# Kernel optimization log

Measured on AMD Instinct MI355X. Metric: run time of the kernel, lower is better.

Reference implementation:

```python
import jax, jax.numpy as jnp
import numpy as np
from jax import lax

B, C, T_IN = 512, 22, 1001   # input width includes the subject-id column
K, KS, P = 40, 25, 100       # num_kernels, kernel_size, pool_size
S, NOUT = 9, 4               # num_subjects, n_outputs
BN_EPS = 1e-5


def setup_inputs() -> dict:
    key = jax.random.key(0)
    ks = jax.random.split(key, 6)
    x = jax.random.normal(ks[0], (B, C, T_IN), dtype=jnp.float32)
    # subject ids in 1..9 encoded as id*1e6 at x[:, 0, -1] (as in the torch module)
    sid = jax.random.randint(ks[1], (B,), 1, S + 1)
    x = x.at[:, 0, -1].set(sid.astype(jnp.float32) * 1e6)
    W = 0.05 * jax.random.normal(ks[2], (S, K, C, KS), dtype=jnp.float32)
    b = 0.05 * jax.random.normal(ks[3], (S, K), dtype=jnp.float32)
    gamma = jnp.ones((K,), dtype=jnp.float32)
    beta = jnp.zeros((K,), dtype=jnp.float32)
    fc_in = K * ((T_IN - 1 - KS + 1) // P)  # 40 * 9 = 360
    fc_w = 0.05 * jax.random.normal(ks[4], (NOUT, fc_in), dtype=jnp.float32)
    fc_b = jnp.zeros((NOUT,), dtype=jnp.float32)
    return {"x": x, "W": W, "b": b, "gamma": gamma, "beta": beta,
            "fc_w": fc_w, "fc_b": fc_b}


def reference(x, W, b, gamma, beta, fc_w, fc_b):
    # decode per-sample subject routing id (0-based into stacked weights)
    sid = (x[:, 0, -1] / 1e6).astype(jnp.int32) - 1        # [B]
    xs = x[:, :, :-1]                                      # [B, C, T]
    Wg = W[sid]                                            # [B, K, C, KS] gathered expert weights
    bg = b[sid]                                            # [B, K]

    # per-sample 1D valid conv with its own expert weights (batched via vmap)
    def conv1(xi, wi):  # xi: [C, T], wi: [K, C, KS]
        return lax.conv_general_dilated(xi[None], wi, (1,), 'VALID',
                                        dimension_numbers=('NCH', 'OIH', 'NCH'))[0]

    y = jax.vmap(conv1)(xs, Wg) + bg[:, :, None]           # [B, K, To]
    y = jax.nn.elu(y)

    # BatchNorm2d in training mode: batch statistics over (B, spatial), biased var
    mean = y.mean(axis=(0, 2))
    var = y.var(axis=(0, 2))
    y = (y - mean[None, :, None]) * (gamma / jnp.sqrt(var + BN_EPS))[None, :, None] \
        + beta[None, :, None]

    # AvgPool over non-overlapping windows of size P (stride = P, floor)
    To = y.shape[-1]
    nw = To // P
    y = y[..., : nw * P].reshape(y.shape[0], K, nw, P).mean(axis=-1)  # [B, K, nw]

    y = y.reshape(y.shape[0], -1)          # [B, K*nw]; dropout is identity in eval
    return y @ fc_w.T + fc_b               # [B, NOUT]
```

## Files before the change

### kernel.cpp

```cpp
#include <hip/hip_runtime.h>
#include <hip/hip_bf16.h>

#define B_ 512
#define C_ 22
#define TIN 1001
#define K_ 40
#define KS_ 25
#define TO 976
#define P_ 100
#define NW 9
#define NOUT 4
#define FCIN 360
#define NBLK 512

#define XTR 1056
#define LDS_TOTAL (XTR * 64)
#define NPAD 48
#define WB_ELEM_S (KS_ * NPAD * 32)

typedef __attribute__((ext_vector_type(8))) short bf16x8;
typedef __attribute__((ext_vector_type(4))) float f32x4;
typedef __attribute__((ext_vector_type(4))) int i32x4;

__device__ __forceinline__ float waveReduceSum(float v) {
#pragma unroll
  for (int m = 32; m >= 1; m >>= 1) v += __shfl_xor(v, m, 64);
  return v;
}

__device__ __forceinline__ unsigned short f2bf(float f) {
  __hip_bfloat16 h = __float2bfloat16(f);
  return *reinterpret_cast<unsigned short*>(&h);
}

__global__ __launch_bounds__(192) void wconv_kernel(const float* __restrict__ W,
                                                    unsigned short* __restrict__ WBg) {
  const int s = blockIdx.x / KS_;
  const int j = blockIdx.x % KS_;
  const int n = threadIdx.x >> 2;
  const int q = threadIdx.x & 3;
  union {
    unsigned short u[8];
    i32x4 v;
  } pk;
#pragma unroll
  for (int e = 0; e < 8; ++e) {
    const int c = q * 8 + e;
    float v = 0.f;
    if (n < K_ && c < C_) v = W[(((size_t)s * K_ + n) * C_ + c) * KS_ + j];
    pk.u[e] = f2bf(v);
  }
  *(i32x4*)(WBg + ((size_t)(s * KS_ + j) * NPAD + n) * 32 + q * 8) = pk.v;
}

#define MFMA24(A, Bv)                                                          \
  do {                                                                         \
    _Pragma("unroll") for (int nt_ = 0; nt_ < 3; ++nt_) {                      \
      _Pragma("unroll") for (int m_ = 0; m_ < 8; ++m_) {                       \
        acc[m_][nt_] =                                                         \
            __builtin_amdgcn_mfma_f32_16x16x32_bf16(A[m_], Bv[nt_], acc[m_][nt_], 0, 0, 0); \
      }                                                                        \
    }                                                                          \
  } while (0)

__global__ __launch_bounds__(512, 2) void conv_kernel(
    const float* __restrict__ x, const unsigned short* __restrict__ WBg,
    const float* __restrict__ bias, float* __restrict__ pooled,
    float* __restrict__ part_sum, float* __restrict__ part_sq) {
  extern __shared__ __align__(16) char sm[];
  const int b = blockIdx.x;
  const int tid = threadIdx.x;

  int s = (int)rintf(x[(size_t)b * (C_ * TIN) + (TIN - 1)] * 1e-6f) - 1;
  s = __builtin_amdgcn_readfirstlane(min(max(s, 0), 8));

  {
    const float* xb = x + (size_t)b * (C_ * TIN);
    for (int task = tid; task < 4 * XTR; task += 512) {
      const int q = task / XTR;
      const int t = task - q * XTR;
      const int lq = q ^ ((t >> 1) & 3);
      union {
        unsigned short u[8];
        i32x4 v;
      } pk;
#pragma unroll
      for (int e = 0; e < 8; ++e) {
        const int c = lq * 8 + e;
        float v = 0.f;
        if (c < C_ && t < TIN - 1) v = xb[c * TIN + t];
        pk.u[e] = f2bf(v);
      }
      *(i32x4*)(sm + t * 64 + q * 16) = pk.v;
    }
  }
  __syncthreads();

  const int lane = tid & 63;
  const int wv = tid >> 6;
  const int l15 = lane & 15;
  const int lg = lane >> 4;
  const int rb = wv * 128;
  const int tb = rb + l15;

  const unsigned short* WBs = WBg + (size_t)s * WB_ELEM_S + (l15 * 32 + lg * 8);

  f32x4 acc[8][3];
#pragma unroll
  for (int m = 0; m < 8; ++m)
#pragma unroll
    for (int nt = 0; nt < 3; ++nt) acc[m][nt] = (f32x4){0.f, 0.f, 0.f, 0.f};

  bf16x8 A0[8], A1[8], B0[3], B1[3];

#define LDA(J, A)                                                              \
  do {                                                                         \
    const int t_ = tb + (J);                                                   \
    const char* ap_ = sm + t_ * 64 + ((lg ^ ((t_ >> 1) & 3)) << 4);            \
    _Pragma("unroll") for (int m_ = 0; m_ < 8; ++m_) {                         \
      A[m_] = *(const bf16x8*)(ap_ + m_ * 1024);                               \
    }                                                                          \
  } while (0)

#define LDB(J, Bv)                                                             \
  do {                                                                         \
    const unsigned short* bp_ = WBs + (size_t)(J)*1536;                        \
    _Pragma("unroll") for (int nt_ = 0; nt_ < 3; ++nt_) {                      \
      Bv[nt_] = *(const bf16x8*)(bp_ + nt_ * 512);                             \
    }                                                                          \
  } while (0)

  LDA(0, A0);
  LDB(0, B0);
  for (int j = 0; j < 24; j += 2) {
    LDA(j + 1, A1);
    LDB(j + 1, B1);
    MFMA24(A0, B0);
    LDA(j + 2, A0);
    LDB(j + 2, B0);
    MFMA24(A1, B1);
  }
  MFMA24(A0, B0);

  float bv[3];
#pragma unroll
  for (int nt = 0; nt < 3; ++nt) {
    const int k = nt * 16 + l15;
    bv[nt] = bias[s * K_ + (k < K_ ? k : 0)];
  }
  const int wlo = rb / P_;
  const int base100 = wlo * P_;
  float sY[3] = {0.f, 0.f, 0.f}, sY2[3] = {0.f, 0.f, 0.f};
  float p0[3] = {0.f, 0.f, 0.f}, p1[3] = {0.f, 0.f, 0.f}, p2[3] = {0.f, 0.f, 0.f};
#pragma unroll
  for (int m = 0; m < 8; ++m) {
#pragma unroll
    for (int i = 0; i < 4; ++i) {
      const int t = rb + m * 16 + lg * 4 + i;
      const bool valid = (t < TO);
      const bool pool = (t < NW * P_);
      const int d = t - base100;
#pragma unroll
      for (int nt = 0; nt < 3; ++nt) {
        const float v = acc[m][nt][i] + bv[nt];
        const float y = v > 0.f ? v : expm1f(v);
        if (valid) {
          sY[nt] += y;
          sY2[nt] += y * y;
          if (pool) {
            if (d < P_)
              p0[nt] += y;
            else if (d < 2 * P_)
              p1[nt] += y;
            else
              p2[nt] += y;
          }
        }
      }
    }
  }
  float* red = (float*)sm;
  __syncthreads();
#pragma unroll
  for (int nt = 0; nt < 3; ++nt) {
#pragma unroll
    for (int r = 16; r <= 32; r <<= 1) {
      p0[nt] += __shfl_xor(p0[nt], r, 64);
      p1[nt] += __shfl_xor(p1[nt], r, 64);
      p2[nt] += __shfl_xor(p2[nt], r, 64);
      sY[nt] += __shfl_xor(sY[nt], r, 64);
      sY2[nt] += __shfl_xor(sY2[nt], r, 64);
    }
    const int k = nt * 16 + l15;
    if (lane < 16 && k < K_) {
      float* pb = pooled + (size_t)b * FCIN + k * NW;
      if (p0[nt] != 0.f) atomicAdd(&pb[wlo], p0[nt]);
      if (wlo + 1 <= NW - 1 && p1[nt] != 0.f) atomicAdd(&pb[wlo + 1], p1[nt]);
      if (wlo + 2 <= NW - 1 && p2[nt] != 0.f) atomicAdd(&pb[wlo + 2], p2[nt]);
      red[k * 8 + wv] = sY[nt];
      red[K_ * 8 + k * 8 + wv] = sY2[nt];
    }
  }
  __syncthreads();
  if (tid < K_) {
    float a = 0.f, q = 0.f;
#pragma unroll
    for (int i = 0; i < 8; ++i) {
      a += red[tid * 8 + i];
      q += red[K_ * 8 + tid * 8 + i];
    }
    part_sum[(size_t)tid * NBLK + b] = a;
    part_sq[(size_t)tid * NBLK + b] = q;
  }
}

__global__ __launch_bounds__(256) void stats_kernel(
    const float* __restrict__ part_sum, const float* __restrict__ part_sq,
    const float* __restrict__ gamma, const float* __restrict__ beta,
    float* __restrict__ ss) {
  const int k = blockIdx.x;
  float s = 0.f, q = 0.f;
  for (int i = threadIdx.x; i < NBLK; i += 256) {
    s += part_sum[(size_t)k * NBLK + i];
    q += part_sq[(size_t)k * NBLK + i];
  }
  s = waveReduceSum(s);
  q = waveReduceSum(q);
  __shared__ float ls[4], lq[4];
  const int wave = threadIdx.x >> 6, lane = threadIdx.x & 63;
  if (lane == 0) {
    ls[wave] = s;
    lq[wave] = q;
  }
  __syncthreads();
  if (threadIdx.x == 0) {
    const float S = ls[0] + ls[1] + ls[2] + ls[3];
    const float Q = lq[0] + lq[1] + lq[2] + lq[3];
    const float N = (float)B_ * (float)TO;
    const float mean = S / N;
    const float var = Q / N - mean * mean;
    const float sc = gamma[k] / sqrtf(var + 1e-5f);
    ss[k] = sc;
    ss[K_ + k] = beta[k] - mean * sc;
  }
}

__global__ __launch_bounds__(256) void fc_kernel(
    const float* __restrict__ pooled, const float* __restrict__ ss,
    const float* __restrict__ fc_w, const float* __restrict__ fc_b,
    float* __restrict__ out) {
  const int bb = blockIdx.x;
  const int n = threadIdx.x >> 6;
  const int lane = threadIdx.x & 63;
  float acc = 0.f;
  for (int i = lane; i < FCIN; i += 64) {
    const int k = i / NW;
    const float y = pooled[(size_t)bb * FCIN + i] * (1.f / (float)P_) * ss[k] + ss[K_ + k];
    acc = fmaf(y, fc_w[n * FCIN + i], acc);
  }
  acc = waveReduceSum(acc);
  if (lane == 0) out[bb * NOUT + n] = acc + fc_b[n];
}

extern "C" void kernel_launch(void* const* d_in, const int* in_sizes, int n_in,
                              void* d_out, int out_size, void* d_ws, size_t ws_size,
                              hipStream_t stream) {
  const float* x = (const float*)d_in[0];
  const float* W = (const float*)d_in[1];
  const float* bias = (const float*)d_in[2];
  const float* gamma = (const float*)d_in[3];
  const float* beta = (const float*)d_in[4];
  const float* fc_w = (const float*)d_in[5];
  const float* fc_b = (const float*)d_in[6];
  float* out = (float*)d_out;

  char* ws = (char*)d_ws;
  float* pooled = (float*)ws;
  float* part_sum = (float*)(ws + 737280);
  float* part_sq = (float*)(ws + 819200);
  unsigned short* WBg = (unsigned short*)(ws + 901120);
  float* ss = (float*)(ws + 1592320);

  hipFuncSetAttribute((const void*)conv_kernel,
                      hipFuncAttributeMaxDynamicSharedMemorySize, LDS_TOTAL);

  hipMemsetAsync(pooled, 0, 737280, stream);
  wconv_kernel<<<9 * KS_, 192, 0, stream>>>(W, WBg);
  conv_kernel<<<NBLK, 512, LDS_TOTAL, stream>>>(x, WBg, bias, pooled, part_sum, part_sq);
  stats_kernel<<<K_, 256, 0, stream>>>(part_sum, part_sq, gamma, beta, ss);
  fc_kernel<<<B_, 256, 0, stream>>>(pooled, ss, fc_w, fc_b, out);
}
```

Baseline: 109.1 us.

## Split each sample's conv across four time-quarter blocks of 256 threads

The conv kernel now launches four blocks per sample instead of one, with each block covering 256 output time steps using 4 waves and a 280-row LDS tile instead of the full 1056-row tile. Each wave holds 4 M-tiles rather than 8, so register use and LDS per block drop and more blocks can be resident per CU, which improves occupancy and load balance across the grid. In exchange the halo rows of x are loaded and converted to bf16 by more than one block, there are more atomic adds into the pooled buffer, and the stats reduction reads four times as many partial sums.

```diff
diff --git a/kernel.cpp b/kernel.cpp
--- a/kernel.cpp
+++ b/kernel.cpp
@@ -11,10 +11,13 @@
 #define NW 9
 #define NOUT 4
 #define FCIN 360
-#define NBLK 512
-
-#define XTR 1056
-#define LDS_TOTAL (XTR * 64)
+
+#define QROWS 280
+#define XT_BYTES (QROWS * 64)
+#define RED_OFF XT_BYTES
+#define RED_BYTES (K_ * 4 * 2 * 4)
+#define LDS_TOTAL (RED_OFF + RED_BYTES)
+#define NBLKQ 2048
 #define NPAD 48
 #define WB_ELEM_S (KS_ * NPAD * 32)
 
@@ -53,22 +56,42 @@
   *(i32x4*)(WBg + ((size_t)(s * KS_ + j) * NPAD + n) * 32 + q * 8) = pk.v;
 }
 
-#define MFMA24(A, Bv)                                                          \
+#define MFMA12(A, Bv)                                                          \
   do {                                                                         \
     _Pragma("unroll") for (int nt_ = 0; nt_ < 3; ++nt_) {                      \
-      _Pragma("unroll") for (int m_ = 0; m_ < 8; ++m_) {                       \
+      _Pragma("unroll") for (int m_ = 0; m_ < 4; ++m_) {                       \
         acc[m_][nt_] =                                                         \
             __builtin_amdgcn_mfma_f32_16x16x32_bf16(A[m_], Bv[nt_], acc[m_][nt_], 0, 0, 0); \
       }                                                                        \
     }                                                                          \
   } while (0)
 
-__global__ __launch_bounds__(512, 2) void conv_kernel(
+#define LDA(J, A)                                                              \
+  do {                                                                         \
+    const int tl_ = tbl + (J);                                                 \
+    const char* ap_ = sm + tl_ * 64 + ((lg ^ ((tl_ >> 1) & 3)) << 4);          \
+    _Pragma("unroll") for (int m_ = 0; m_ < 4; ++m_) {                         \
+      A[m_] = *(const bf16x8*)(ap_ + m_ * 1024);                               \
+    }                                                                          \
+  } while (0)
+
+#define LDB(J, Bv)                                                             \
+  do {                                                                         \
+    const unsigned short* bp_ = WBs + (J) * 1536;                              \
+    _Pragma("unroll") for (int nt_ = 0; nt_ < 3; ++nt_) {                      \
+      Bv[nt_] = *(const bf16x8*)(bp_ + nt_ * 512);                             \
+    }                                                                          \
+  } while (0)
+
+__global__ __launch_bounds__(256, 4) void conv_kernel(
     const float* __restrict__ x, const unsigned short* __restrict__ WBg,
     const float* __restrict__ bias, float* __restrict__ pooled,
     float* __restrict__ part_sum, float* __restrict__ part_sq) {
   extern __shared__ __align__(16) char sm[];
-  const int b = blockIdx.x;
+  const int blk = blockIdx.x;
+  const int b = blk >> 2;
+  const int p = blk & 3;
+  const int rbg = p * 256;
   const int tid = threadIdx.x;
 
   int s = (int)rintf(x[(size_t)b * (C_ * TIN) + (TIN - 1)] * 1e-6f) - 1;
@@ -76,10 +99,11 @@
 
   {
     const float* xb = x + (size_t)b * (C_ * TIN);
-    for (int task = tid; task < 4 * XTR; task += 512) {
-      const int q = task / XTR;
-      const int t = task - q * XTR;
-      const int lq = q ^ ((t >> 1) & 3);
+    for (int task = tid; task < 4 * QROWS; task += 256) {
+      const int q = task / QROWS;
+      const int tr = task - q * QROWS;
+      const int lq = q ^ ((tr >> 1) & 3);
+      const int tg = rbg + tr;
       union {
         unsigned short u[8];
         i32x4 v;
@@ -88,10 +112,10 @@
       for (int e = 0; e < 8; ++e) {
         const int c = lq * 8 + e;
         float v = 0.f;
-        if (c < C_ && t < TIN - 1) v = xb[c * TIN + t];
+        if (c < C_ && tg < TIN - 1) v = xb[c * TIN + tg];
         pk.u[e] = f2bf(v);
       }
-      *(i32x4*)(sm + t * 64 + q * 16) = pk.v;
+      *(i32x4*)(sm + tr * 64 + q * 16) = pk.v;
     }
   }
   __syncthreads();
@@ -100,47 +124,29 @@
   const int wv = tid >> 6;
   const int l15 = lane & 15;
   const int lg = lane >> 4;
-  const int rb = wv * 128;
-  const int tb = rb + l15;
+  const int tbl = wv * 64 + l15;
 
   const unsigned short* WBs = WBg + (size_t)s * WB_ELEM_S + (l15 * 32 + lg * 8);
 
-  f32x4 acc[8][3];
-#pragma unroll
-  for (int m = 0; m < 8; ++m)
+  f32x4 acc[4][3];
+#pragma unroll
+  for (int m = 0; m < 4; ++m)
 #pragma unroll
     for (int nt = 0; nt < 3; ++nt) acc[m][nt] = (f32x4){0.f, 0.f, 0.f, 0.f};
 
-  bf16x8 A0[8], A1[8], B0[3], B1[3];
-
-#define LDA(J, A)                                                              \
-  do {                                                                         \
-    const int t_ = tb + (J);                                                   \
-    const char* ap_ = sm + t_ * 64 + ((lg ^ ((t_ >> 1) & 3)) << 4);            \
-    _Pragma("unroll") for (int m_ = 0; m_ < 8; ++m_) {                         \
-      A[m_] = *(const bf16x8*)(ap_ + m_ * 1024);                               \
-    }                                                                          \
-  } while (0)
-
-#define LDB(J, Bv)                                                             \
-  do {                                                                         \
-    const unsigned short* bp_ = WBs + (size_t)(J)*1536;                        \
-    _Pragma("unroll") for (int nt_ = 0; nt_ < 3; ++nt_) {                      \
-      Bv[nt_] = *(const bf16x8*)(bp_ + nt_ * 512);                             \
-    }                                                                          \
-  } while (0)
+  bf16x8 A0[4], A1[4], B0[3], B1[3];
 
   LDA(0, A0);
   LDB(0, B0);
   for (int j = 0; j < 24; j += 2) {
     LDA(j + 1, A1);
     LDB(j + 1, B1);
-    MFMA24(A0, B0);
+    MFMA12(A0, B0);
     LDA(j + 2, A0);
     LDB(j + 2, B0);
-    MFMA24(A1, B1);
-  }
-  MFMA24(A0, B0);
+    MFMA12(A1, B1);
+  }
+  MFMA12(A0, B0);
 
   float bv[3];
 #pragma unroll
@@ -148,15 +154,20 @@
     const int k = nt * 16 + l15;
     bv[nt] = bias[s * K_ + (k < K_ ? k : 0)];
   }
-  const int wlo = rb / P_;
-  const int base100 = wlo * P_;
+  const int wbase = rbg / P_;
+  const int base100 = wbase * P_;
   float sY[3] = {0.f, 0.f, 0.f}, sY2[3] = {0.f, 0.f, 0.f};
-  float p0[3] = {0.f, 0.f, 0.f}, p1[3] = {0.f, 0.f, 0.f}, p2[3] = {0.f, 0.f, 0.f};
-#pragma unroll
-  for (int m = 0; m < 8; ++m) {
+  float pw[4][3];
+#pragma unroll
+  for (int w4 = 0; w4 < 4; ++w4)
+#pragma unroll
+    for (int nt = 0; nt < 3; ++nt) pw[w4][nt] = 0.f;
+
+#pragma unroll
+  for (int m = 0; m < 4; ++m) {
 #pragma unroll
     for (int i = 0; i < 4; ++i) {
-      const int t = rb + m * 16 + lg * 4 + i;
+      const int t = rbg + wv * 64 + m * 16 + lg * 4 + i;
       const bool valid = (t < TO);
       const bool pool = (t < NW * P_);
       const int d = t - base100;
@@ -169,48 +180,53 @@
           sY2[nt] += y * y;
           if (pool) {
             if (d < P_)
-              p0[nt] += y;
+              pw[0][nt] += y;
             else if (d < 2 * P_)
-              p1[nt] += y;
+              pw[1][nt] += y;
+            else if (d < 3 * P_)
+              pw[2][nt] += y;
             else
-              p2[nt] += y;
+              pw[3][nt] += y;
           }
         }
       }
     }
   }
-  float* red = (float*)sm;
-  __syncthreads();
+
+  float* red = (float*)(sm + RED_OFF);
 #pragma unroll
   for (int nt = 0; nt < 3; ++nt) {
 #pragma unroll
     for (int r = 16; r <= 32; r <<= 1) {
-      p0[nt] += __shfl_xor(p0[nt], r, 64);
-      p1[nt] += __shfl_xor(p1[nt], r, 64);
-      p2[nt] += __shfl_xor(p2[nt], r, 64);
+      pw[0][nt] += __shfl_xor(pw[0][nt], r, 64);
+      pw[1][nt] += __shfl_xor(pw[1][nt], r, 64);
+      pw[2][nt] += __shfl_xor(pw[2][nt], r, 64);
+      pw[3][nt] += __shfl_xor(pw[3][nt], r, 64);
       sY[nt] += __shfl_xor(sY[nt], r, 64);
       sY2[nt] += __shfl_xor(sY2[nt], r, 64);
     }
     const int k = nt * 16 + l15;
     if (lane < 16 && k < K_) {
       float* pb = pooled + (size_t)b * FCIN + k * NW;
-      if (p0[nt] != 0.f) atomicAdd(&pb[wlo], p0[nt]);
-      if (wlo + 1 <= NW - 1 && p1[nt] != 0.f) atomicAdd(&pb[wlo + 1], p1[nt]);
-      if (wlo + 2 <= NW - 1 && p2[nt] != 0.f) atomicAdd(&pb[wlo + 2], p2[nt]);
-      red[k * 8 + wv] = sY[nt];
-      red[K_ * 8 + k * 8 + wv] = sY2[nt];
+#pragma unroll
+      for (int w4 = 0; w4 < 4; ++w4) {
+        const int wg = wbase + w4;
+        if (wg <= NW - 1 && pw[w4][nt] != 0.f) atomicAdd(&pb[wg], pw[w4][nt]);
+      }
+      red[k * 4 + wv] = sY[nt];
+      red[K_ * 4 + k * 4 + wv] = sY2[nt];
     }
   }
   __syncthreads();
   if (tid < K_) {
     float a = 0.f, q = 0.f;
 #pragma unroll
-    for (int i = 0; i < 8; ++i) {
-      a += red[tid * 8 + i];
-      q += red[K_ * 8 + tid * 8 + i];
-    }
-    part_sum[(size_t)tid * NBLK + b] = a;
-    part_sq[(size_t)tid * NBLK + b] = q;
+    for (int i = 0; i < 4; ++i) {
+      a += red[tid * 4 + i];
+      q += red[K_ * 4 + tid * 4 + i];
+    }
+    part_sum[(size_t)tid * NBLKQ + blk] = a;
+    part_sq[(size_t)tid * NBLKQ + blk] = q;
   }
 }
 
@@ -220,9 +236,9 @@
     float* __restrict__ ss) {
   const int k = blockIdx.x;
   float s = 0.f, q = 0.f;
-  for (int i = threadIdx.x; i < NBLK; i += 256) {
-    s += part_sum[(size_t)k * NBLK + i];
-    q += part_sq[(size_t)k * NBLK + i];
+  for (int i = threadIdx.x; i < NBLKQ; i += 256) {
+    s += part_sum[(size_t)k * NBLKQ + i];
+    q += part_sq[(size_t)k * NBLKQ + i];
   }
   s = waveReduceSum(s);
   q = waveReduceSum(q);
@@ -277,16 +293,16 @@
   char* ws = (char*)d_ws;
   float* pooled = (float*)ws;
   float* part_sum = (float*)(ws + 737280);
-  float* part_sq = (float*)(ws + 819200);
-  unsigned short* WBg = (unsigned short*)(ws + 901120);
-  float* ss = (float*)(ws + 1592320);
+  float* part_sq = (float*)(ws + 1064960);
+  unsigned short* WBg = (unsigned short*)(ws + 1392640);
+  float* ss = (float*)(ws + 2083840);
 
   hipFuncSetAttribute((const void*)conv_kernel,
                       hipFuncAttributeMaxDynamicSharedMemorySize, LDS_TOTAL);
 
   hipMemsetAsync(pooled, 0, 737280, stream);
   wconv_kernel<<<9 * KS_, 192, 0, stream>>>(W, WBg);
-  conv_kernel<<<NBLK, 512, LDS_TOTAL, stream>>>(x, WBg, bias, pooled, part_sum, part_sq);
+  conv_kernel<<<NBLKQ, 256, LDS_TOTAL, stream>>>(x, WBg, bias, pooled, part_sum, part_sq);
   stats_kernel<<<K_, 256, 0, stream>>>(part_sum, part_sq, gamma, beta, ss);
   fc_kernel<<<B_, 256, 0, stream>>>(pooled, ss, fc_w, fc_b, out);
 }
```

Result: faster. 106.8 us (-2.1%).
